# Kernel optimization log

Hardware: AMD Instinct MI355X
Metric: run time of the kernel (lower is better)

The kernel has to match this reference:

```python
import jax, jax.numpy as jnp
import numpy as np

P = 16          # patch size
NUM_HEADS = 8
WINDOW = 64     # window_size from SparseAttention(window_size=64)


def _layer_norm(x, w, b, eps=1e-5):
    mu = jnp.mean(x, axis=-1, keepdims=True)
    var = jnp.var(x, axis=-1, keepdims=True)
    return (x - mu) * jax.lax.rsqrt(var + eps) * w + b


def _sinusoidal_pe(num_patches, num_features, dtype):
    pos = jnp.arange(num_patches, dtype=jnp.float32)[:, None]            # [N,1]
    i = jnp.arange(0, num_features, 2, dtype=jnp.float32)                # [D/2]
    div = jnp.exp(-jnp.log(10000.0) * i / num_features)                  # [D/2]
    ang = pos * div                                                      # [N,D/2]
    pe = jnp.stack([jnp.sin(ang), jnp.cos(ang)], axis=-1).reshape(num_patches, num_features)
    return pe.astype(dtype)


def _ffn(x, w1, b1, w2, b2):
    # FeedForward: Linear -> GELU -> Linear (dropout inactive at eval)
    h = jax.nn.gelu(jnp.einsum('bnd,hd->bnh', x, w1) + b1)
    return jnp.einsum('bnh,dh->bnd', h, w2) + b2


def _windowed_attention(x, qkv_w, qkv_b, proj_w, proj_b):
    B, N, D = x.shape
    hd = D // NUM_HEADS
    qkv = jnp.einsum('bnd,ed->bne', x, qkv_w) + qkv_b                    # [B,N,3D]
    qkv = qkv.reshape(B, N, 3, NUM_HEADS, hd)
    q, k, v = qkv[:, :, 0], qkv[:, :, 1], qkv[:, :, 2]                   # [B,N,H,hd]
    nw = N // WINDOW
    # partition sequence into non-overlapping windows of 64 tokens
    q = q.reshape(B, nw, WINDOW, NUM_HEADS, hd).transpose(0, 3, 1, 2, 4)  # [B,H,nw,W,hd]
    k = k.reshape(B, nw, WINDOW, NUM_HEADS, hd).transpose(0, 3, 1, 2, 4)
    v = v.reshape(B, nw, WINDOW, NUM_HEADS, hd).transpose(0, 3, 1, 2, 4)
    scale = 1.0 / jnp.sqrt(jnp.asarray(hd, x.dtype))
    scores = jnp.einsum('bhwqd,bhwkd->bhwqk', q, k) * scale              # [B,H,nw,W,W]
    attn = jax.nn.softmax(scores, axis=-1)
    out = jnp.einsum('bhwqk,bhwkd->bhwqd', attn, v)                      # [B,H,nw,W,hd]
    out = out.transpose(0, 2, 3, 1, 4).reshape(B, N, D)
    return jnp.einsum('bnd,ed->bne', out, proj_w) + proj_b


def setup_inputs() -> dict:
    key = jax.random.key(0)
    ks = jax.random.split(key, 8)
    D, HF = 256, 1024
    s = lambda fan: 1.0 / np.sqrt(fan)
    return {
        'x': jax.random.normal(ks[0], (32, 3, 512, 512), jnp.float32),
        'conv_w': jax.random.normal(ks[1], (D, 3, P, P), jnp.float32) * s(3 * P * P),
        'conv_b': jnp.zeros((D,), jnp.float32),
        'ln_w': jnp.ones((D,), jnp.float32),
        'ln_b': jnp.zeros((D,), jnp.float32),
        'qkv_w': jax.random.normal(ks[2], (3 * D, D), jnp.float32) * s(D),
        'qkv_b': jnp.zeros((3 * D,), jnp.float32),
        'proj_w': jax.random.normal(ks[3], (D, D), jnp.float32) * s(D),
        'proj_b': jnp.zeros((D,), jnp.float32),
        'ff_w1': jax.random.normal(ks[4], (HF, D), jnp.float32) * s(D),
        'ff_b1': jnp.zeros((HF,), jnp.float32),
        'ff_w2': jax.random.normal(ks[5], (D, HF), jnp.float32) * s(HF),
        'ff_b2': jnp.zeros((D,), jnp.float32),
    }


def reference(x, conv_w, conv_b, ln_w, ln_b, qkv_w, qkv_b, proj_w, proj_b,
              ff_w1, ff_b1, ff_w2, ff_b2):
    B, C, H, W = x.shape
    D = conv_w.shape[0]
    # PatchEmbedding1: Conv2d(C, D, kernel=16, stride=16) == per-patch matmul, then LayerNorm
    nH, nW = H // P, W // P
    patches = x.reshape(B, C, nH, P, nW, P).transpose(0, 2, 4, 1, 3, 5).reshape(B, nH * nW, C * P * P)
    h = jnp.einsum('bnp,dp->bnd', patches, conv_w.reshape(D, -1)) + conv_b
    h = _layer_norm(h, ln_w, ln_b)
    # static sinusoidal position embedding
    h = h + _sinusoidal_pe(h.shape[1], D, h.dtype)
    # block 1: FFN -> sparse (windowed) attention -> residual
    identity = h
    h = _ffn(h, ff_w1, ff_b1, ff_w2, ff_b2)
    h = _windowed_attention(h, qkv_w, qkv_b, proj_w, proj_b)
    h = h + identity
    # block 2: shared FFN -> residual
    identity = h
    h = _ffn(h, ff_w1, ff_b1, ff_w2, ff_b2)
    return h + identity
```

## Files before the change

kernel.cpp:

```cpp
#include <hip/hip_runtime.h>
#include <math.h>


#define M_TOK 32768

typedef __attribute__((ext_vector_type(8))) short  short8;
typedef __attribute__((ext_vector_type(4))) float  f32x4;
typedef __attribute__((ext_vector_type(8))) unsigned short us8v;
typedef __attribute__((ext_vector_type(4))) unsigned short us4v;

__device__ __forceinline__ unsigned short f2b(float f) {
    union { float f; unsigned u; } c; c.f = f;
    unsigned r = c.u + 0x7fffu + ((c.u >> 16) & 1u);
    return (unsigned short)(r >> 16);
}
__device__ __forceinline__ float gelu_fast(float x) {
    const float c0 = 0.7978845608028654f;
    const float c1 = 0.044715f * 0.7978845608028654f;
    float z = x * (c0 + c1 * x * x);
    float e = __expf(-2.0f * z);
    return x * __builtin_amdgcn_rcpf(1.0f + e);
}
__device__ __forceinline__ void load_lds16(const unsigned short* g, void* lds) {
    __builtin_amdgcn_global_load_lds(
        (const __attribute__((address_space(1))) unsigned int*)g,
        (__attribute__((address_space(3))) unsigned int*)lds, 16, 0, 0);
}

__global__ __launch_bounds__(256) void cvt_weights_kernel(
    const float* __restrict__ s0, const float* __restrict__ s1,
    const float* __restrict__ s2, const float* __restrict__ s3,
    const float* __restrict__ s4,
    unsigned short* __restrict__ d0, unsigned short* __restrict__ d1,
    unsigned short* __restrict__ d2, unsigned short* __restrict__ d3,
    unsigned short* __restrict__ d4)
{
    const int bid = blockIdx.x;
    const float* src; unsigned short* dst; int off;
    if      (bid < 192) { src = s0; dst = d0; off = bid; }
    else if (bid < 384) { src = s1; dst = d1; off = bid - 192; }
    else if (bid < 448) { src = s2; dst = d2; off = bid - 384; }
    else if (bid < 704) { src = s3; dst = d3; off = bid - 448; }
    else                { src = s4; dst = d4; off = bid - 704; }
    const int i = off * 1024 + threadIdx.x * 4;
    float4 v = *(const float4*)(src + i);
    us4v o;
    o[0] = f2b(v.x); o[1] = f2b(v.y); o[2] = f2b(v.z); o[3] = f2b(v.w);
    *(us4v*)(dst + i) = o;
}

__global__ __launch_bounds__(256) void pe_init_kernel(float* __restrict__ pe)
{
    const int pos = blockIdx.x;
    const int d   = threadIdx.x;
    const int ieven = d & ~1;
    float div = expf(-9.210340371976184f * (float)ieven * (1.0f / 256.0f));
    float ang = (float)pos * div;
    pe[pos * 256 + d] = (d & 1) ? cosf(ang) : sinf(ang);
}

template<bool GELU, bool RES, bool WF32, bool WB16>
__global__ __launch_bounds__(512) void mfma_gemm_kernel(
    const unsigned short* __restrict__ A, const unsigned short* __restrict__ W,
    const float* __restrict__ bias, const float* __restrict__ res,
    float* __restrict__ outF, unsigned short* __restrict__ outB,
    int M, int N, int K)
{
    __shared__ unsigned short As[2 * 128 * 64];
    __shared__ unsigned short Ws[2 * 128 * 64];

    const int t    = threadIdx.x;
    const int m0   = blockIdx.x * 128;
    const int n0   = blockIdx.y * 128;
    const int wv   = t >> 6, lane = t & 63;
    const int wr   = (wv >> 2) * 64;
    const int wc   = (wv & 3) * 32;
    const int l15  = lane & 15, quad = lane >> 4;

    f32x4 acc[4][2];
#pragma unroll
    for (int i = 0; i < 4; i++)
#pragma unroll
        for (int j = 0; j < 2; j++)
#pragma unroll
            for (int r = 0; r < 4; r++) acc[i][j][r] = 0.0f;

    const int srow = wv * 8 + (lane >> 3);
    const int skk  = (((lane & 7) ^ ((lane >> 3) & 7)) * 8);
    const unsigned short* gA = A + (size_t)(m0 + srow) * K + skk;
    const unsigned short* gW = W + (size_t)(n0 + srow) * K + skk;
    char* lA = (char*)As + wv * 1024;
    char* lW = (char*)Ws + wv * 1024;

    const int cswz = (l15 & 7) * 8;
    const int nt   = K >> 6;

#define GSTAGE(tt, BUFOFF)                                                     \
    {                                                                          \
        const int kk = (tt) << 6;                                              \
        _Pragma("unroll")                                                      \
        for (int s = 0; s < 2; s++) {                                          \
            load_lds16(gA + (size_t)(s * 64) * K + kk, lA + (BUFOFF) + s * 8192); \
            load_lds16(gW + (size_t)(s * 64) * K + kk, lW + (BUFOFF) + s * 8192); \
        }                                                                      \
    }

#define GCOMPUTE(BUFOFF)                                                       \
    {                                                                          \
        const unsigned short* Ab = (const unsigned short*)((const char*)As + (BUFOFF)); \
        const unsigned short* Wb = (const unsigned short*)((const char*)Ws + (BUFOFF)); \
        _Pragma("unroll")                                                      \
        for (int kh = 0; kh < 2; kh++) {                                       \
            const int coff = (kh * 32 + quad * 8) ^ cswz;                      \
            short8 af[4], wf[2];                                               \
            _Pragma("unroll")                                                  \
            for (int i = 0; i < 4; i++)                                        \
                af[i] = *(const short8*)&Ab[(wr + i * 16 + l15) * 64 + coff];  \
            _Pragma("unroll")                                                  \
            for (int j = 0; j < 2; j++)                                        \
                wf[j] = *(const short8*)&Wb[(wc + j * 16 + l15) * 64 + coff];  \
            _Pragma("unroll")                                                  \
            for (int i = 0; i < 4; i++)                                        \
                _Pragma("unroll")                                              \
                for (int j = 0; j < 2; j++)                                    \
                    acc[i][j] = __builtin_amdgcn_mfma_f32_16x16x32_bf16(       \
                        af[i], wf[j], acc[i][j], 0, 0, 0);                     \
        }                                                                      \
    }

    GSTAGE(0, 0);
    for (int tt = 0; tt < nt; tt += 2) {
        GSTAGE(tt + 1, 16384);
        asm volatile("s_waitcnt vmcnt(4)" ::: "memory");
        __builtin_amdgcn_s_barrier();
        __builtin_amdgcn_sched_barrier(0);
        GCOMPUTE(0);
        __builtin_amdgcn_s_barrier();
        if (tt + 2 < nt) {
            GSTAGE(tt + 2, 0);
            asm volatile("s_waitcnt vmcnt(4)" ::: "memory");
        } else {
            asm volatile("s_waitcnt vmcnt(0)" ::: "memory");
        }
        __builtin_amdgcn_s_barrier();
        __builtin_amdgcn_sched_barrier(0);
        GCOMPUTE(16384);
        __builtin_amdgcn_s_barrier();
    }
#undef GSTAGE
#undef GCOMPUTE

#pragma unroll
    for (int i = 0; i < 4; i++) {
        const int gr = m0 + wr + i * 16 + quad * 4;
#pragma unroll
        for (int j = 0; j < 2; j++) {
            const int gc = n0 + wc + j * 16 + l15;
            const float bv = bias[gc];
#pragma unroll
            for (int r = 0; r < 4; r++) {
                float v = acc[i][j][r] + bv;
                if (GELU) v = gelu_fast(v);
                if (RES)  v += res[(size_t)(gr + r) * N + gc];
                if (WF32) outF[(size_t)(gr + r) * N + gc] = v;
                if (WB16) outB[(size_t)(gr + r) * N + gc] = f2b(v);
            }
        }
    }
}

__global__ __launch_bounds__(512) void patch_fused_kernel(
    const float* __restrict__ x, const unsigned short* __restrict__ W,
    const float* __restrict__ bias, float* __restrict__ outF)
{
    __shared__ unsigned short As[2 * 128 * 64];
    __shared__ unsigned short Ws[2 * 256 * 64];

    const int t    = threadIdx.x;
    const int m0   = blockIdx.x * 128;
    const int wv   = t >> 6, lane = t & 63;
    const int wr   = (wv >> 2) * 64;
    const int wc   = (wv & 3) * 64;
    const int l15  = lane & 15, quad = lane >> 4;

    f32x4 acc[4][4];
#pragma unroll
    for (int i = 0; i < 4; i++)
#pragma unroll
        for (int j = 0; j < 4; j++)
#pragma unroll
            for (int r = 0; r < 4; r++) acc[i][j][r] = 0.0f;

    const int ar  = t >> 2;
    const int ac0 = (t & 3) * 16;
    const int am  = m0 + ar;
    const int ab  = am >> 10;
    const int ahh = (am >> 5) & 31;
    const int aww = am & 31;
    const float* axbase = x + (size_t)ab * 786432 + (size_t)ahh * 8192 + aww * 16;
    const int alc = ac0 >> 3;
    char* aw0 = (char*)As + ar * 128 + ((alc    ) ^ (ar & 7)) * 16;
    char* aw1 = (char*)As + ar * 128 + ((alc + 1) ^ (ar & 7)) * 16;

    const int wsrow = wv * 8 + (lane >> 3);
    const int wskk  = (((lane & 7) ^ ((lane >> 3) & 7)) * 8);
    const unsigned short* gW = W + (size_t)wsrow * 768 + wskk;
    char* lW = (char*)Ws + wv * 1024;

    const int cswz = (l15 & 7) * 8;

    float4 av0, av1, av2, av3;

#define PA_ISSUE(tt)                                                           \
    {                                                                          \
        const int k0 = ((tt) << 6) + ac0;                                      \
        const int c  = k0 >> 8;                                                \
        const int ph = (k0 >> 4) & 15;                                         \
        const float* s = axbase + (size_t)c * 262144 + ph * 512;               \
        av0 = *(const float4*)(s);                                             \
        av1 = *(const float4*)(s + 4);                                         \
        av2 = *(const float4*)(s + 8);                                         \
        av3 = *(const float4*)(s + 12);                                        \
    }
#define PA_WRITE(BUFOFF)                                                       \
    {                                                                          \
        us8v o0, o1;                                                           \
        o0[0] = f2b(av0.x); o0[1] = f2b(av0.y); o0[2] = f2b(av0.z); o0[3] = f2b(av0.w); \
        o0[4] = f2b(av1.x); o0[5] = f2b(av1.y); o0[6] = f2b(av1.z); o0[7] = f2b(av1.w); \
        o1[0] = f2b(av2.x); o1[1] = f2b(av2.y); o1[2] = f2b(av2.z); o1[3] = f2b(av2.w); \
        o1[4] = f2b(av3.x); o1[5] = f2b(av3.y); o1[6] = f2b(av3.z); o1[7] = f2b(av3.w); \
        *(us8v*)(aw0 + (BUFOFF)) = o0;                                         \
        *(us8v*)(aw1 + (BUFOFF)) = o1;                                         \
    }
#define PW_ISSUE(tt, BUFOFF)                                                   \
    {                                                                          \
        const int kk = (tt) << 6;                                              \
        _Pragma("unroll")                                                      \
        for (int s = 0; s < 4; s++)                                            \
            load_lds16(gW + (size_t)(s * 64) * 768 + kk, lW + (BUFOFF) + s * 8192); \
    }
#define PCOMPUTE(AOFF, WOFF)                                                   \
    {                                                                          \
        const unsigned short* Ab = (const unsigned short*)((const char*)As + (AOFF)); \
        const unsigned short* Wb = (const unsigned short*)((const char*)Ws + (WOFF)); \
        _Pragma("unroll")                                                      \
        for (int kh = 0; kh < 2; kh++) {                                       \
            const int coff = (kh * 32 + quad * 8) ^ cswz;                      \
            short8 af[4], wf[4];                                               \
            _Pragma("unroll")                                                  \
            for (int i = 0; i < 4; i++)                                        \
                af[i] = *(const short8*)&Ab[(wr + i * 16 + l15) * 64 + coff];  \
            _Pragma("unroll")                                                  \
            for (int j = 0; j < 4; j++)                                        \
                wf[j] = *(const short8*)&Wb[(wc + j * 16 + l15) * 64 + coff];  \
            _Pragma("unroll")                                                  \
            for (int i = 0; i < 4; i++)                                        \
                _Pragma("unroll")                                              \
                for (int j = 0; j < 4; j++)                                    \
                    acc[i][j] = __builtin_amdgcn_mfma_f32_16x16x32_bf16(       \
                        af[i], wf[j], acc[i][j], 0, 0, 0);                     \
        }                                                                      \
    }

    PA_ISSUE(0);
    PW_ISSUE(0, 0);
    asm volatile("s_waitcnt vmcnt(0)" ::: "memory");
    PA_WRITE(0);
    asm volatile("s_waitcnt lgkmcnt(0)" ::: "memory");
    __builtin_amdgcn_s_barrier();
    __builtin_amdgcn_sched_barrier(0);

    for (int tt = 0; tt < 12; ++tt) {
        const int aoff_c = (tt & 1) * 16384;
        const int woff_c = (tt & 1) * 32768;
        if (tt < 11) {
            PA_ISSUE(tt + 1);
            PW_ISSUE(tt + 1, woff_c ^ 32768);
        }
        PCOMPUTE(aoff_c, woff_c);
        if (tt < 11) {
            asm volatile("s_waitcnt vmcnt(0)" ::: "memory");
            PA_WRITE(aoff_c ^ 16384);
            asm volatile("s_waitcnt lgkmcnt(0)" ::: "memory");
            __builtin_amdgcn_s_barrier();
            __builtin_amdgcn_sched_barrier(0);
        }
    }
#undef PA_ISSUE
#undef PA_WRITE
#undef PW_ISSUE
#undef PCOMPUTE

#pragma unroll
    for (int i = 0; i < 4; i++) {
        const int gr = m0 + wr + i * 16 + quad * 4;
#pragma unroll
        for (int j = 0; j < 4; j++) {
            const int gc = wc + j * 16 + l15;
            const float bv = bias[gc];
#pragma unroll
            for (int r = 0; r < 4; r++)
                outF[(size_t)(gr + r) * 256 + gc] = acc[i][j][r] + bv;
        }
    }
}

__global__ __launch_bounds__(256) void ln_pe_kernel(
    const float* __restrict__ in, const float* __restrict__ w,
    const float* __restrict__ b, const float* __restrict__ pe_t,
    float* __restrict__ outF, unsigned short* __restrict__ outB)
{
    const int m = blockIdx.x;
    const int d = threadIdx.x;
    float v = in[(size_t)m * 256 + d];

    float s = v, s2 = v * v;
#pragma unroll
    for (int off = 32; off > 0; off >>= 1) {
        s  += __shfl_down(s,  off, 64);
        s2 += __shfl_down(s2, off, 64);
    }
    __shared__ float ss[4], ss2[4], stats[2];
    const int lane = d & 63, wid = d >> 6;
    if (lane == 0) { ss[wid] = s; ss2[wid] = s2; }
    __syncthreads();
    if (d == 0) {
        float a  = ss[0] + ss[1] + ss[2] + ss[3];
        float a2 = ss2[0] + ss2[1] + ss2[2] + ss2[3];
        float mean = a * (1.0f / 256.0f);
        float var  = a2 * (1.0f / 256.0f) - mean * mean;
        stats[0] = mean;
        stats[1] = rsqrtf(var + 1e-5f);
    }
    __syncthreads();
    const float mean = stats[0], rstd = stats[1];

    const int pos = m & 1023;
    float pe = pe_t[pos * 256 + d];

    float o = (v - mean) * rstd * w[d] + b[d] + pe;
    outF[(size_t)m * 256 + d] = o;
    outB[(size_t)m * 256 + d] = f2b(o);
}

__global__ __launch_bounds__(256) void attn_mfma_kernel(
    const unsigned short* __restrict__ qkv, unsigned short* __restrict__ out)
{
    __shared__ unsigned short Ps[64 * 72];
    __shared__ unsigned short Vt[32 * 72];

    const int blk = blockIdx.x;
    const int h = blk & 7;
    const int w = (blk >> 3) & 15;
    const int b = blk >> 7;
    const int m_base = b * 1024 + w * 64;

    const int t = threadIdx.x;
    const int wv = t >> 6, lane = t & 63;
    const int l15 = lane & 15, quad = lane >> 4;

    {
        const int row = t >> 2;
        const int c0  = (t & 3) * 8;
        const unsigned short* src = qkv + (size_t)(m_base + row) * 768 + 512 + h * 32 + c0;
        us8v v = *(const us8v*)src;
#pragma unroll
        for (int j = 0; j < 8; j++) Vt[(c0 + j) * 72 + row] = v[j];
    }

    short8 aq = *(const short8*)(qkv + (size_t)(m_base + wv * 16 + l15) * 768 + h * 32 + quad * 8);
    f32x4 c[4];
#pragma unroll
    for (int j = 0; j < 4; j++) {
        short8 bk = *(const short8*)(qkv + (size_t)(m_base + j * 16 + l15) * 768 + 256 + h * 32 + quad * 8);
        f32x4 z = {0.0f, 0.0f, 0.0f, 0.0f};
        c[j] = __builtin_amdgcn_mfma_f32_16x16x32_bf16(aq, bk, z, 0, 0, 0);
    }

    const float scale = 0.17677669529663687f;
    float sm[4];
#pragma unroll
    for (int r = 0; r < 4; r++) {
        float m0 = -1e30f;
#pragma unroll
        for (int j = 0; j < 4; j++) { c[j][r] *= scale; m0 = fmaxf(m0, c[j][r]); }
#pragma unroll
        for (int d = 1; d < 16; d <<= 1) m0 = fmaxf(m0, __shfl_xor(m0, d, 64));
        float s0 = 0.0f;
#pragma unroll
        for (int j = 0; j < 4; j++) { float e = __expf(c[j][r] - m0); c[j][r] = e; s0 += e; }
#pragma unroll
        for (int d = 1; d < 16; d <<= 1) s0 += __shfl_xor(s0, d, 64);
        sm[r] = __builtin_amdgcn_rcpf(s0);
    }

#pragma unroll
    for (int r = 0; r < 4; r++) {
        const int prow = wv * 16 + quad * 4 + r;
#pragma unroll
        for (int j = 0; j < 4; j++)
            Ps[prow * 72 + j * 16 + l15] = f2b(c[j][r] * sm[r]);
    }
    __syncthreads();

    short8 ap0 = *(const short8*)&Ps[(wv * 16 + l15) * 72 + quad * 8];
    short8 ap1 = *(const short8*)&Ps[(wv * 16 + l15) * 72 + 32 + quad * 8];
    f32x4 o[2];
#pragma unroll
    for (int nt = 0; nt < 2; nt++) {
        short8 bv0 = *(const short8*)&Vt[(nt * 16 + l15) * 72 + quad * 8];
        short8 bv1 = *(const short8*)&Vt[(nt * 16 + l15) * 72 + 32 + quad * 8];
        f32x4 z = {0.0f, 0.0f, 0.0f, 0.0f};
        o[nt] = __builtin_amdgcn_mfma_f32_16x16x32_bf16(ap0, bv0, z, 0, 0, 0);
        o[nt] = __builtin_amdgcn_mfma_f32_16x16x32_bf16(ap1, bv1, o[nt], 0, 0, 0);
    }

#pragma unroll
    for (int nt = 0; nt < 2; nt++) {
#pragma unroll
        for (int r = 0; r < 4; r++) {
            const int row = m_base + wv * 16 + quad * 4 + r;
            out[(size_t)row * 256 + h * 32 + nt * 16 + l15] = f2b(o[nt][r]);
        }
    }
}

extern "C" void kernel_launch(void* const* d_in, const int* in_sizes, int n_in,
                              void* d_out, int out_size, void* d_ws, size_t ws_size,
                              hipStream_t stream)
{
    const float* x      = (const float*)d_in[0];
    const float* conv_w = (const float*)d_in[1];
    const float* conv_b = (const float*)d_in[2];
    const float* ln_w   = (const float*)d_in[3];
    const float* ln_b   = (const float*)d_in[4];
    const float* qkv_w  = (const float*)d_in[5];
    const float* qkv_b  = (const float*)d_in[6];
    const float* proj_w = (const float*)d_in[7];
    const float* proj_b = (const float*)d_in[8];
    const float* ff_w1  = (const float*)d_in[9];
    const float* ff_b1  = (const float*)d_in[10];
    const float* ff_w2  = (const float*)d_in[11];
    const float* ff_b2  = (const float*)d_in[12];
    float* out = (float*)d_out;

    char* ws = (char*)d_ws;
    unsigned short* hidb  = (unsigned short*)(ws);
    float*          h0    = (float*)(ws + 67108864);
    unsigned short* qkvb  = (unsigned short*)(ws + 67108864);
    float*          pe_t  = (float*)(ws + 100663296);
    float*          h1f   = (float*)(ws + 117440512);
    unsigned short* h1b   = (unsigned short*)(ws + 150994944);
    unsigned short* aob   = (unsigned short*)(ws + 150994944);
    unsigned short* f1b   = (unsigned short*)(ws + 167772160);
    unsigned short* h2b   = (unsigned short*)(ws + 167772160);
    unsigned short* wbase = (unsigned short*)(ws + 184549376);
    unsigned short* conv_wb = wbase;
    unsigned short* qkv_wb  = wbase + 196608;
    unsigned short* proj_wb = wbase + 393216;
    unsigned short* ff_w1b  = wbase + 458752;
    unsigned short* ff_w2b  = wbase + 720896;

    const int M = M_TOK;
    dim3 blk(256);
    dim3 blk512(512);

    cvt_weights_kernel<<<dim3(960), blk, 0, stream>>>(
        conv_w, qkv_w, proj_w, ff_w1, ff_w2,
        conv_wb, qkv_wb, proj_wb, ff_w1b, ff_w2b);
    pe_init_kernel<<<dim3(1024), blk, 0, stream>>>(pe_t);

    patch_fused_kernel<<<dim3(M / 128), blk512, 0, stream>>>(x, conv_wb, conv_b, h0);
    ln_pe_kernel<<<dim3(M), blk, 0, stream>>>(h0, ln_w, ln_b, pe_t, h1f, h1b);
    mfma_gemm_kernel<true, false, false, true><<<dim3(M / 128, 8), blk512, 0, stream>>>(
        h1b, ff_w1b, ff_b1, nullptr, nullptr, hidb, M, 1024, 256);
    mfma_gemm_kernel<false, false, false, true><<<dim3(M / 128, 2), blk512, 0, stream>>>(
        hidb, ff_w2b, ff_b2, nullptr, nullptr, f1b, M, 256, 1024);
    mfma_gemm_kernel<false, false, false, true><<<dim3(M / 128, 6), blk512, 0, stream>>>(
        f1b, qkv_wb, qkv_b, nullptr, nullptr, qkvb, M, 768, 256);
    attn_mfma_kernel<<<dim3(4096), blk, 0, stream>>>(qkvb, aob);
    mfma_gemm_kernel<false, true, true, true><<<dim3(M / 128, 2), blk512, 0, stream>>>(
        aob, proj_wb, proj_b, h1f, out, h2b, M, 256, 256);
    mfma_gemm_kernel<true, false, false, true><<<dim3(M / 128, 8), blk512, 0, stream>>>(
        h2b, ff_w1b, ff_b1, nullptr, nullptr, hidb, M, 1024, 256);
    mfma_gemm_kernel<false, true, true, false><<<dim3(M / 128, 2), blk512, 0, stream>>>(
        hidb, ff_w2b, ff_b2, out, out, nullptr, M, 256, 1024);
}
```

Before: 389.0 us.

## Fuse FFN up-projection, GELU and down-projection into one kernel

Adds a fused FFN kernel in which each 128-row block keeps its input tile in LDS. It computes the 1024-wide hidden layer in chunks of 128 columns with GELU, stores each chunk as bf16 in LDS, and accumulates the down-projection in registers. This removes the round trip of the 32768x1024 bf16 hidden activation through global memory and saves two kernel launches per FFN. In exchange, weights are read directly from global memory with no LDS staging, only 256 blocks are launched, and LDS use is high, so occupancy and latency hiding may suffer.

```diff
diff --git a/kernel.cpp b/kernel.cpp
--- a/kernel.cpp
+++ b/kernel.cpp
@@ -169,6 +169,140 @@
     }
 }
 
+template<bool RES, bool WF32, bool WB16>
+__global__ __launch_bounds__(512) void ffn_fused_kernel(
+    const unsigned short* __restrict__ A,  const unsigned short* __restrict__ W1,
+    const float* __restrict__ b1,          const unsigned short* __restrict__ W2,
+    const float* __restrict__ b2,          const float* __restrict__ res,
+    float* __restrict__ outF,              unsigned short* __restrict__ outB)
+{
+    __shared__ unsigned short As[128 * 256];
+    __shared__ unsigned short Hs[128 * 128];
+
+    const int t    = threadIdx.x;
+    const int m0   = blockIdx.x * 128;
+    const int wv   = t >> 6, lane = t & 63;
+    const int wr   = (wv >> 2) * 64;
+    const int wc1  = (wv & 3) * 32;
+    const int wc2  = (wv & 3) * 64;
+    const int l15  = lane & 15, quad = lane >> 4;
+
+    f32x4 oacc[4][4];
+#pragma unroll
+    for (int i = 0; i < 4; i++)
+#pragma unroll
+        for (int j = 0; j < 4; j++)
+#pragma unroll
+            for (int r = 0; r < 4; r++) oacc[i][j][r] = 0.0f;
+
+    {
+        const int arow = wv * 2 + (lane >> 5);
+        const int alc  = (lane & 31) ^ arow;
+        const unsigned short* gA = A + (size_t)(m0 + arow) * 256 + alc * 8;
+        char* lA = (char*)As + wv * 1024;
+#pragma unroll
+        for (int s = 0; s < 8; s++)
+            load_lds16(gA + s * 4096, lA + s * 8192);
+    }
+    asm volatile("s_waitcnt vmcnt(0)" ::: "memory");
+    __builtin_amdgcn_s_barrier();
+
+    const unsigned short* w1p = W1 + (size_t)(wc1 + l15) * 256 + quad * 8;
+    const unsigned short* w2p = W2 + (size_t)(wc2 + l15) * 1024 + quad * 8;
+
+    const int hwc  = (wc1 >> 3) + (quad >> 1);
+    const int hwh  = (quad & 1) * 8;
+
+    for (int c = 0; c < 8; ++c) {
+        f32x4 hacc[4][2];
+#pragma unroll
+        for (int i = 0; i < 4; i++)
+#pragma unroll
+            for (int j = 0; j < 2; j++)
+#pragma unroll
+                for (int r = 0; r < 4; r++) hacc[i][j][r] = 0.0f;
+
+#pragma unroll
+        for (int kc = 0; kc < 8; ++kc) {
+            short8 af[4], wf[2];
+#pragma unroll
+            for (int i = 0; i < 4; i++)
+                af[i] = *(const short8*)&As[(wr + i * 16 + l15) * 256 +
+                                            (((kc * 4 + quad) ^ l15) * 8)];
+#pragma unroll
+            for (int j = 0; j < 2; j++)
+                wf[j] = *(const short8*)(w1p + (size_t)c * 32768 + j * 4096 + kc * 32);
+#pragma unroll
+            for (int i = 0; i < 4; i++)
+#pragma unroll
+                for (int j = 0; j < 2; j++)
+                    hacc[i][j] = __builtin_amdgcn_mfma_f32_16x16x32_bf16(
+                        wf[j], af[i], hacc[i][j], 0, 0, 0);
+        }
+
+        __syncthreads();
+#pragma unroll
+        for (int j = 0; j < 2; j++) {
+            const f32x4 bb = *(const f32x4*)(b1 + c * 128 + wc1 + j * 16 + quad * 4);
+#pragma unroll
+            for (int i = 0; i < 4; i++) {
+                us4v hv;
+#pragma unroll
+                for (int r = 0; r < 4; r++)
+                    hv[r] = f2b(gelu_fast(hacc[i][j][r] + bb[r]));
+                const int m = wr + i * 16 + l15;
+                char* dst = (char*)Hs + m * 256 +
+                            (((hwc + j * 2) ^ l15) << 4) + hwh;
+                *(us4v*)dst = hv;
+            }
+        }
+        __syncthreads();
+
+#pragma unroll
+        for (int kc = 0; kc < 4; ++kc) {
+            short8 ah[4], wf2[4];
+#pragma unroll
+            for (int i = 0; i < 4; i++)
+                ah[i] = *(const short8*)&Hs[(wr + i * 16 + l15) * 128 +
+                                            (((kc * 4 + quad) ^ l15) * 8)];
+#pragma unroll
+            for (int j = 0; j < 4; j++)
+                wf2[j] = *(const short8*)(w2p + j * 16384 + c * 128 + kc * 32);
+#pragma unroll
+            for (int i = 0; i < 4; i++)
+#pragma unroll
+                for (int j = 0; j < 4; j++)
+                    oacc[i][j] = __builtin_amdgcn_mfma_f32_16x16x32_bf16(
+                        wf2[j], ah[i], oacc[i][j], 0, 0, 0);
+        }
+    }
+
+#pragma unroll
+    for (int j = 0; j < 4; j++) {
+        const int n0 = wc2 + j * 16 + quad * 4;
+        const f32x4 bb = *(const f32x4*)(b2 + n0);
+#pragma unroll
+        for (int i = 0; i < 4; i++) {
+            const size_t row = (size_t)(m0 + wr + i * 16 + l15) * 256 + n0;
+            f32x4 v;
+#pragma unroll
+            for (int r = 0; r < 4; r++) v[r] = oacc[i][j][r] + bb[r];
+            if (RES) {
+                const f32x4 rr = *(const f32x4*)(res + row);
+#pragma unroll
+                for (int r = 0; r < 4; r++) v[r] += rr[r];
+            }
+            if (WF32) *(f32x4*)(outF + row) = v;
+            if (WB16) {
+                us4v o;
+#pragma unroll
+                for (int r = 0; r < 4; r++) o[r] = f2b(v[r]);
+                *(us4v*)(outB + row) = o;
+            }
+        }
+    }
+}
+
 __global__ __launch_bounds__(512) void patch_fused_kernel(
     const float* __restrict__ x, const unsigned short* __restrict__ W,
     const float* __restrict__ bias, float* __restrict__ outF)
@@ -445,7 +579,6 @@
     float* out = (float*)d_out;
 
     char* ws = (char*)d_ws;
-    unsigned short* hidb  = (unsigned short*)(ws);
     float*          h0    = (float*)(ws + 67108864);
     unsigned short* qkvb  = (unsigned short*)(ws + 67108864);
     float*          pe_t  = (float*)(ws + 100663296);
@@ -472,17 +605,13 @@
 
     patch_fused_kernel<<<dim3(M / 128), blk512, 0, stream>>>(x, conv_wb, conv_b, h0);
     ln_pe_kernel<<<dim3(M), blk, 0, stream>>>(h0, ln_w, ln_b, pe_t, h1f, h1b);
-    mfma_gemm_kernel<true, false, false, true><<<dim3(M / 128, 8), blk512, 0, stream>>>(
-        h1b, ff_w1b, ff_b1, nullptr, nullptr, hidb, M, 1024, 256);
-    mfma_gemm_kernel<false, false, false, true><<<dim3(M / 128, 2), blk512, 0, stream>>>(
-        hidb, ff_w2b, ff_b2, nullptr, nullptr, f1b, M, 256, 1024);
+    ffn_fused_kernel<false, false, true><<<dim3(M / 128), blk512, 0, stream>>>(
+        h1b, ff_w1b, ff_b1, ff_w2b, ff_b2, nullptr, nullptr, f1b);
     mfma_gemm_kernel<false, false, false, true><<<dim3(M / 128, 6), blk512, 0, stream>>>(
         f1b, qkv_wb, qkv_b, nullptr, nullptr, qkvb, M, 768, 256);
     attn_mfma_kernel<<<dim3(4096), blk, 0, stream>>>(qkvb, aob);
     mfma_gemm_kernel<false, true, true, true><<<dim3(M / 128, 2), blk512, 0, stream>>>(
         aob, proj_wb, proj_b, h1f, out, h2b, M, 256, 256);
-    mfma_gemm_kernel<true, false, false, true><<<dim3(M / 128, 8), blk512, 0, stream>>>(
-        h2b, ff_w1b, ff_b1, nullptr, nullptr, hidb, M, 1024, 256);
-    mfma_gemm_kernel<false, true, true, false><<<dim3(M / 128, 2), blk512, 0, stream>>>(
-        hidb, ff_w2b, ff_b2, out, out, nullptr, M, 256, 1024);
-}
+    ffn_fused_kernel<true, true, false><<<dim3(M / 128), blk512, 0, stream>>>(
+        h2b, ff_w1b, ff_b1, ff_w2b, ff_b2, out, out, nullptr);
+}
```

Result: slower. 444.6 us (+14.3%).
